# Kernel tuning notes

Hardware: AMD Instinct MI355X
Metric: run time of the kernel (lower is better)

## Reference

```python
import jax, jax.numpy as jnp
import numpy as np

B = 4096
N_PATCH = 196  # (28/2)^2


def _rx(theta):
    # theta [...] -> RX matrix [..., 2, 2] complex64
    c = jnp.cos(theta / 2) + 0j
    s = -1j * jnp.sin(theta / 2)
    return jnp.stack([jnp.stack([c, s], -1), jnp.stack([s, c], -1)], -2).astype(jnp.complex64)


def _rot(phi, theta, omega):
    # PennyLane Rot(phi, theta, omega) = RZ(omega) RY(theta) RZ(phi), returns [2,2] complex64
    ct = jnp.cos(theta / 2)
    st = jnp.sin(theta / 2)
    m00 = jnp.exp(-1j * (phi + omega) / 2) * ct
    m01 = -jnp.exp(1j * (phi - omega) / 2) * st
    m10 = jnp.exp(-1j * (phi - omega) / 2) * st
    m11 = jnp.exp(1j * (phi + omega) / 2) * ct
    return jnp.stack([jnp.stack([m00, m01]), jnp.stack([m10, m11])]).astype(jnp.complex64)


def _apply_shared(state, U, w):
    # state [N,2,2,2,2], U [2,2] shared across batch, acting on wire w
    s = jnp.moveaxis(state, 1 + w, -1)
    s = jnp.einsum('...a,ba->...b', s, U)
    return jnp.moveaxis(s, -1, 1 + w)


def _apply_batched(state, U, w):
    # U [N,2,2] per-sample gate
    s = jnp.moveaxis(state, 1 + w, -1)
    s = jnp.einsum('n...a,nba->n...b', s, U)
    return jnp.moveaxis(s, -1, 1 + w)


def _cnot(state, c, t):
    s = jnp.moveaxis(state, (1 + c, 1 + t), (-2, -1))
    s = jnp.stack([s[..., 0, :], s[..., 1, ::-1]], axis=-2)
    return jnp.moveaxis(s, (-2, -1), (1 + c, 1 + t))


def _quanv(patches, wq):
    # patches [N,4] angles; wq [n_app, n_layers, 4, 3]
    N = patches.shape[0]
    state = jnp.zeros((N, 16), jnp.complex64).at[:, 0].set(1.0).reshape(N, 2, 2, 2, 2)
    for w in range(4):  # AngleEmbedding: RX per wire
        state = _apply_batched(state, _rx(patches[:, w]), w)
    ranges = (1, 2)  # SEL default: (l % (n_wires-1)) + 1
    for app in range(wq.shape[0]):
        for l in range(wq.shape[1]):
            for w in range(4):
                state = _apply_shared(state, _rot(wq[app, l, w, 0], wq[app, l, w, 1], wq[app, l, w, 2]), w)
            r = ranges[l]
            for w in range(4):
                state = _cnot(state, w, (w + r) % 4)
    p = jnp.abs(state) ** 2  # [N,2,2,2,2]
    feats = []
    for w in range(4):  # <Z_w> = P(bit_w=0) - P(bit_w=1)
        axes = tuple(a for a in range(1, 5) if a != 1 + w)
        m = p.sum(axes)
        feats.append(m[:, 0] - m[:, 1])
    return jnp.stack(feats, -1)  # [N,4]


def _qfc(params, wfc):
    # 1-qubit circuit: RX embedding then Rot gates only (SEL has no entanglers on 1 wire)
    Bq = params.shape[0]
    state = jnp.zeros((Bq, 2), jnp.complex64).at[:, 0].set(1.0)
    state = jnp.einsum('na,nba->nb', state, _rx(params[:, 0]))
    for app in range(wfc.shape[0]):
        for l in range(wfc.shape[1]):
            U = _rot(wfc[app, l, 0, 0], wfc[app, l, 0, 1], wfc[app, l, 0, 2])
            state = jnp.einsum('na,ba->nb', state, U)
    p = jnp.abs(state) ** 2
    return p[:, 0] - p[:, 1]  # [B]


def setup_inputs() -> dict:
    key = jax.random.key(0)
    k1, k2, k3, k4 = jax.random.split(key, 4)
    return {
        'x': jax.random.normal(k1, (B, 784), jnp.float32),
        'weights_q': jax.random.normal(k2, (2, 2, 4, 3), jnp.float32),
        'weights_fc': jax.random.normal(k3, (3, 3, 1, 3), jnp.float32),
        'W_out': jax.random.normal(k4, (10, 1), jnp.float32) * 0.1,
        'b_out': jnp.zeros((10,), jnp.float32),
    }


def reference(x, weights_q, weights_fc, W_out, b_out):
    Bb = x.shape[0]
    img = x.reshape(Bb, 28, 28)
    # extract 2x2 stride-2 patches in (row-block, col-block) order, row-major within patch
    patches = img.reshape(Bb, 14, 2, 14, 2).transpose(0, 1, 3, 2, 4).reshape(Bb * N_PATCH, 4)
    feats = _quanv(patches, weights_q).reshape(Bb, N_PATCH * 4)  # [B,784]
    q = _qfc(feats[:, :1], weights_fc)  # [B]
    logits = q[:, None] @ W_out.T + b_out  # Linear(1,10) -> [B,10]
    return jax.nn.log_softmax(logits, axis=-1)
```

## Files before the change

kernel.cpp:

```cpp
#include <hip/hip_runtime.h>
#include <math.h>


struct c32 { float re, im; };

__device__ __forceinline__ c32 cmul(c32 a, c32 b) {
    return { fmaf(a.re, b.re, -a.im * b.im), fmaf(a.re, b.im, a.im * b.re) };
}
__device__ __forceinline__ c32 cadd(c32 a, c32 b) { return { a.re + b.re, a.im + b.im }; }

template<int W>
__device__ __forceinline__ void apply1(c32 amp[16], c32 u00, c32 u01, c32 u10, c32 u11) {
    constexpr int s = 8 >> W;
    #pragma unroll
    for (int i = 0; i < 16; ++i) {
        if (i & s) continue;
        c32 a = amp[i], b = amp[i + s];
        amp[i]     = cadd(cmul(u00, a), cmul(u01, b));
        amp[i + s] = cadd(cmul(u10, a), cmul(u11, b));
    }
}

template<int C, int T>
__device__ __forceinline__ void cnot4(c32 amp[16]) {
    constexpr int sc = 8 >> C, st = 8 >> T;
    #pragma unroll
    for (int i = 0; i < 16; ++i) {
        if ((i & sc) && !(i & st)) {
            c32 tmp = amp[i]; amp[i] = amp[i | st]; amp[i | st] = tmp;
        }
    }
}

__device__ __forceinline__ void make_rot(float phi, float th, float om,
                                         c32& u00, c32& u01, c32& u10, c32& u11) {
    float sh, ch; sincosf(th * 0.5f, &sh, &ch);
    float spo, cpo; sincosf((phi + om) * 0.5f, &spo, &cpo);
    float spm, cpm; sincosf((phi - om) * 0.5f, &spm, &cpm);
    u00 = {  cpo * ch, -spo * ch };
    u01 = { -cpm * sh, -spm * sh };
    u10 = {  cpm * sh, -spm * sh };
    u11 = {  cpo * ch,  spo * ch };
}

template<int W>
__device__ __forceinline__ void rx_apply(c32 amp[16], float ang) {
    float s, c; sincosf(ang * 0.5f, &s, &c);
    apply1<W>(amp, c32{c, 0.f}, c32{0.f, -s}, c32{0.f, -s}, c32{c, 0.f});
}

template<int W>
__device__ __forceinline__ void rot_apply(c32 amp[16], const float* p) {
    c32 a, b, c, d;
    make_rot(p[0], p[1], p[2], a, b, c, d);
    apply1<W>(amp, a, b, c, d);
}

__global__ __launch_bounds__(64)
void quanv_hybrid_kernel(const float* __restrict__ x,
                         const float* __restrict__ wq,
                         const float* __restrict__ wfc,
                         const float* __restrict__ Wout,
                         const float* __restrict__ bout,
                         float* __restrict__ out,
                         int B)
{
    int b = blockIdx.x * blockDim.x + threadIdx.x;
    if (b >= B) return;

    const float* xb = x + (size_t)b * 784;
    float ang0 = xb[0], ang1 = xb[1], ang2 = xb[28], ang3 = xb[29];

    c32 amp[16];
    #pragma unroll
    for (int i = 0; i < 16; ++i) amp[i] = { 0.f, 0.f };
    amp[0].re = 1.f;

    rx_apply<0>(amp, ang0);
    rx_apply<1>(amp, ang1);
    rx_apply<2>(amp, ang2);
    rx_apply<3>(amp, ang3);

    #pragma unroll
    for (int al = 0; al < 4; ++al) {
        const float* wp = wq + al * 12;
        rot_apply<0>(amp, wp + 0);
        rot_apply<1>(amp, wp + 3);
        rot_apply<2>(amp, wp + 6);
        rot_apply<3>(amp, wp + 9);
        if ((al & 1) == 0) {
            cnot4<0,1>(amp); cnot4<1,2>(amp); cnot4<2,3>(amp); cnot4<3,0>(amp);
        } else {
            cnot4<0,2>(amp); cnot4<1,3>(amp); cnot4<2,0>(amp); cnot4<3,1>(amp);
        }
    }

    float p0 = 0.f, p1 = 0.f;
    #pragma unroll
    for (int i = 0; i < 16; ++i) {
        float p = fmaf(amp[i].re, amp[i].re, amp[i].im * amp[i].im);
        if (i < 8) p0 += p; else p1 += p;
    }
    float z0 = p0 - p1;

    float sh, chh; sincosf(z0 * 0.5f, &sh, &chh);
    c32 psi0 = { chh, 0.f }, psi1 = { 0.f, -sh };
    #pragma unroll
    for (int g = 0; g < 9; ++g) {
        const float* p = wfc + g * 3;
        c32 u00, u01, u10, u11;
        make_rot(p[0], p[1], p[2], u00, u01, u10, u11);
        c32 n0 = cadd(cmul(u00, psi0), cmul(u01, psi1));
        c32 n1 = cadd(cmul(u10, psi0), cmul(u11, psi1));
        psi0 = n0; psi1 = n1;
    }
    float q = (psi0.re * psi0.re + psi0.im * psi0.im)
            - (psi1.re * psi1.re + psi1.im * psi1.im);

    float lg[10], m = -1e30f;
    #pragma unroll
    for (int j = 0; j < 10; ++j) {
        lg[j] = fmaf(q, Wout[j], bout[j]);
        m = fmaxf(m, lg[j]);
    }
    float sum = 0.f;
    #pragma unroll
    for (int j = 0; j < 10; ++j) sum += expf(lg[j] - m);
    float lse = m + logf(sum);

    float* ob = out + (size_t)b * 10;
    #pragma unroll
    for (int j = 0; j < 10; ++j) ob[j] = lg[j] - lse;
}

extern "C" void kernel_launch(void* const* d_in, const int* in_sizes, int n_in,
                              void* d_out, int out_size, void* d_ws, size_t ws_size,
                              hipStream_t stream) {
    const float* x    = (const float*)d_in[0];
    const float* wq   = (const float*)d_in[1];
    const float* wfc  = (const float*)d_in[2];
    const float* Wout = (const float*)d_in[3];
    const float* bout = (const float*)d_in[4];
    float* out = (float*)d_out;

    int B = in_sizes[0] / 784;
    const int threads = 64;
    int blocks = (B + threads - 1) / threads;
    quanv_hybrid_kernel<<<blocks, threads, 0, stream>>>(x, wq, wfc, Wout, bout, out, B);
}
```

Before: 86.21 us.

## Precompute circuit observable as Pauli-basis coefficients and evaluate per-sample polynomial

Each block first builds the 16x16 unitary of the weight layers in shared memory. It then forms the Z0 observable conjugated by that unitary, expands it into 81 Pauli-product coefficients, and collapses the 9-gate FC circuit into two scalars. Each sample now evaluates a small trigonometric polynomial in its four RX angles instead of simulating the full 16-amplitude state, which removes most of the per-sample complex arithmetic. In exchange every block recomputes the precomputation and adds three barriers, with block size raised to 256 threads.

```diff
diff --git a/kernel.cpp b/kernel.cpp
--- a/kernel.cpp
+++ b/kernel.cpp
@@ -8,29 +8,7 @@
     return { fmaf(a.re, b.re, -a.im * b.im), fmaf(a.re, b.im, a.im * b.re) };
 }
 __device__ __forceinline__ c32 cadd(c32 a, c32 b) { return { a.re + b.re, a.im + b.im }; }
-
-template<int W>
-__device__ __forceinline__ void apply1(c32 amp[16], c32 u00, c32 u01, c32 u10, c32 u11) {
-    constexpr int s = 8 >> W;
-    #pragma unroll
-    for (int i = 0; i < 16; ++i) {
-        if (i & s) continue;
-        c32 a = amp[i], b = amp[i + s];
-        amp[i]     = cadd(cmul(u00, a), cmul(u01, b));
-        amp[i + s] = cadd(cmul(u10, a), cmul(u11, b));
-    }
-}
-
-template<int C, int T>
-__device__ __forceinline__ void cnot4(c32 amp[16]) {
-    constexpr int sc = 8 >> C, st = 8 >> T;
-    #pragma unroll
-    for (int i = 0; i < 16; ++i) {
-        if ((i & sc) && !(i & st)) {
-            c32 tmp = amp[i]; amp[i] = amp[i | st]; amp[i | st] = tmp;
-        }
-    }
-}
+__device__ __forceinline__ c32 conjc(c32 a) { return { a.re, -a.im }; }
 
 __device__ __forceinline__ void make_rot(float phi, float th, float om,
                                          c32& u00, c32& u01, c32& u10, c32& u11) {
@@ -44,9 +22,26 @@
 }
 
 template<int W>
-__device__ __forceinline__ void rx_apply(c32 amp[16], float ang) {
-    float s, c; sincosf(ang * 0.5f, &s, &c);
-    apply1<W>(amp, c32{c, 0.f}, c32{0.f, -s}, c32{0.f, -s}, c32{c, 0.f});
+__device__ __forceinline__ void apply1(c32 amp[16], c32 u00, c32 u01, c32 u10, c32 u11) {
+    constexpr int s = 8 >> W;
+    #pragma unroll
+    for (int i = 0; i < 16; ++i) {
+        if (i & s) continue;
+        c32 a = amp[i], b = amp[i + s];
+        amp[i]     = cadd(cmul(u00, a), cmul(u01, b));
+        amp[i + s] = cadd(cmul(u10, a), cmul(u11, b));
+    }
+}
+
+template<int C, int T>
+__device__ __forceinline__ void cnot4(c32 amp[16]) {
+    constexpr int sc = 8 >> C, st = 8 >> T;
+    #pragma unroll
+    for (int i = 0; i < 16; ++i) {
+        if ((i & sc) && !(i & st)) {
+            c32 tmp = amp[i]; amp[i] = amp[i | st]; amp[i | st] = tmp;
+        }
+    }
 }
 
 template<int W>
@@ -56,7 +51,7 @@
     apply1<W>(amp, a, b, c, d);
 }
 
-__global__ __launch_bounds__(64)
+__global__ __launch_bounds__(256)
 void quanv_hybrid_kernel(const float* __restrict__ x,
                          const float* __restrict__ wq,
                          const float* __restrict__ wfc,
@@ -65,68 +60,142 @@
                          float* __restrict__ out,
                          int B)
 {
-    int b = blockIdx.x * blockDim.x + threadIdx.x;
+    __shared__ c32 U[16][16];
+    __shared__ c32 M[16][16];
+    __shared__ float mc[81];
+    __shared__ float fc_beta, fc_gamma;
+
+    const int tid = threadIdx.x;
+
+    if (tid < 16) {
+        c32 amp[16];
+        #pragma unroll
+        for (int i = 0; i < 16; ++i) amp[i] = { 0.f, 0.f };
+        amp[tid].re = 1.f;
+        #pragma unroll
+        for (int al = 0; al < 4; ++al) {
+            const float* wp = wq + al * 12;
+            rot_apply<0>(amp, wp + 0);
+            rot_apply<1>(amp, wp + 3);
+            rot_apply<2>(amp, wp + 6);
+            rot_apply<3>(amp, wp + 9);
+            if ((al & 1) == 0) {
+                cnot4<0,1>(amp); cnot4<1,2>(amp); cnot4<2,3>(amp); cnot4<3,0>(amp);
+            } else {
+                cnot4<0,2>(amp); cnot4<1,3>(amp); cnot4<2,0>(amp); cnot4<3,1>(amp);
+            }
+        }
+        #pragma unroll
+        for (int k = 0; k < 16; ++k) U[k][tid] = amp[k];
+    }
+
+    if (tid == 64) {
+        c32 v00 = {1.f,0.f}, v01 = {0.f,0.f}, v10 = {0.f,0.f}, v11 = {1.f,0.f};
+        #pragma unroll
+        for (int g = 0; g < 9; ++g) {
+            const float* p = wfc + g * 3;
+            c32 u00, u01, u10, u11;
+            make_rot(p[0], p[1], p[2], u00, u01, u10, u11);
+            c32 n00 = cadd(cmul(u00, v00), cmul(u01, v10));
+            c32 n01 = cadd(cmul(u00, v01), cmul(u01, v11));
+            c32 n10 = cadd(cmul(u10, v00), cmul(u11, v10));
+            c32 n11 = cadd(cmul(u10, v01), cmul(u11, v11));
+            v00 = n00; v01 = n01; v10 = n10; v11 = n11;
+        }
+        fc_beta  = (v00.re*v00.re + v00.im*v00.im) - (v10.re*v10.re + v10.im*v10.im);
+        c32 h01 = cadd(cmul(conjc(v00), v01),
+                       c32{ -(conjc(v10).re*v11.re - conjc(v10).im*v11.im),
+                            -(conjc(v10).re*v11.im + conjc(v10).im*v11.re) });
+        fc_gamma = h01.im;
+    }
+    __syncthreads();
+
+    {
+        const int i = tid >> 4, j = tid & 15;
+        c32 s = {0.f, 0.f};
+        #pragma unroll
+        for (int k = 0; k < 16; ++k) {
+            c32 t = cmul(conjc(U[k][i]), U[k][j]);
+            if (k < 8) { s.re += t.re; s.im += t.im; }
+            else       { s.re -= t.re; s.im -= t.im; }
+        }
+        M[i][j] = s;
+    }
+    __syncthreads();
+
+    if (tid < 81) {
+        const int t = tid;
+        int d[4] = { t / 27, (t / 9) % 3, (t / 3) % 3, t % 3 };
+        int xmask = 0;
+        #pragma unroll
+        for (int w = 0; w < 4; ++w) if (d[w] == 1) xmask |= (8 >> w);
+        float acc = 0.f;
+        float acci = 0.f;
+        for (int i = 0; i < 16; ++i) {
+            const int j = i ^ xmask;
+            float pre = 1.f, pim = 0.f;
+            #pragma unroll
+            for (int w = 0; w < 4; ++w) {
+                const int b = (i >> (3 - w)) & 1;
+                if (d[w] == 2) {
+                    if (b) { pre = -pre; pim = -pim; }
+                } else if (d[w] == 1) {
+                    float nre = b ? -pim :  pim;
+                    float nim = b ?  pre : -pre;
+                    pre = nre; pim = nim;
+                }
+            }
+            c32 m = M[j][i];
+            acc  += pre * m.re - pim * m.im;
+            acci += pre * m.im + pim * m.re;
+            (void)acci;
+        }
+        mc[t] = acc * (1.f / 16.f);
+    }
+    __syncthreads();
+
+    const int b = blockIdx.x * 256 + tid;
     if (b >= B) return;
 
     const float* xb = x + (size_t)b * 784;
-    float ang0 = xb[0], ang1 = xb[1], ang2 = xb[28], ang3 = xb[29];
-
-    c32 amp[16];
-    #pragma unroll
-    for (int i = 0; i < 16; ++i) amp[i] = { 0.f, 0.f };
-    amp[0].re = 1.f;
-
-    rx_apply<0>(amp, ang0);
-    rx_apply<1>(amp, ang1);
-    rx_apply<2>(amp, ang2);
-    rx_apply<3>(amp, ang3);
-
-    #pragma unroll
-    for (int al = 0; al < 4; ++al) {
-        const float* wp = wq + al * 12;
-        rot_apply<0>(amp, wp + 0);
-        rot_apply<1>(amp, wp + 3);
-        rot_apply<2>(amp, wp + 6);
-        rot_apply<3>(amp, wp + 9);
-        if ((al & 1) == 0) {
-            cnot4<0,1>(amp); cnot4<1,2>(amp); cnot4<2,3>(amp); cnot4<3,0>(amp);
-        } else {
-            cnot4<0,2>(amp); cnot4<1,3>(amp); cnot4<2,0>(amp); cnot4<3,1>(amp);
-        }
-    }
-
-    float p0 = 0.f, p1 = 0.f;
-    #pragma unroll
-    for (int i = 0; i < 16; ++i) {
-        float p = fmaf(amp[i].re, amp[i].re, amp[i].im * amp[i].im);
-        if (i < 8) p0 += p; else p1 += p;
-    }
-    float z0 = p0 - p1;
-
-    float sh, chh; sincosf(z0 * 0.5f, &sh, &chh);
-    c32 psi0 = { chh, 0.f }, psi1 = { 0.f, -sh };
-    #pragma unroll
-    for (int g = 0; g < 9; ++g) {
-        const float* p = wfc + g * 3;
-        c32 u00, u01, u10, u11;
-        make_rot(p[0], p[1], p[2], u00, u01, u10, u11);
-        c32 n0 = cadd(cmul(u00, psi0), cmul(u01, psi1));
-        c32 n1 = cadd(cmul(u10, psi0), cmul(u11, psi1));
-        psi0 = n0; psi1 = n1;
-    }
-    float q = (psi0.re * psi0.re + psi0.im * psi0.im)
-            - (psi1.re * psi1.re + psi1.im * psi1.im);
-
-    float lg[10], m = -1e30f;
+    const float a0 = xb[0], a1 = xb[1], a2 = xb[28], a3 = xb[29];
+
+    float u0[3], u1[3], u2[3], u3[3];
+    { float s, c; sincosf(a0, &s, &c); u0[0]=1.f; u0[1]=-s; u0[2]=c; }
+    { float s, c; sincosf(a1, &s, &c); u1[0]=1.f; u1[1]=-s; u1[2]=c; }
+    { float s, c; sincosf(a2, &s, &c); u2[0]=1.f; u2[1]=-s; u2[2]=c; }
+    { float s, c; sincosf(a3, &s, &c); u3[0]=1.f; u3[1]=-s; u3[2]=c; }
+
+    float z0 = 0.f;
+    #pragma unroll
+    for (int t0 = 0; t0 < 3; ++t0) {
+        float s1 = 0.f;
+        #pragma unroll
+        for (int t1 = 0; t1 < 3; ++t1) {
+            float s2 = 0.f;
+            #pragma unroll
+            for (int t2 = 0; t2 < 3; ++t2) {
+                const float* m = &mc[((t0 * 3 + t1) * 3 + t2) * 3];
+                s2 = fmaf(m[0] + fmaf(m[1], u3[1], 0.f) + m[2] * u3[2], u2[t2], s2);
+            }
+            s1 = fmaf(s2, u1[t1], s1);
+        }
+        z0 = fmaf(s1, u0[t0], z0);
+    }
+
+    float sz, cz; sincosf(z0, &sz, &cz);
+    const float q = fmaf(fc_beta, cz, fc_gamma * sz);
+
+    float lg[10], mx = -1e30f;
     #pragma unroll
     for (int j = 0; j < 10; ++j) {
         lg[j] = fmaf(q, Wout[j], bout[j]);
-        m = fmaxf(m, lg[j]);
+        mx = fmaxf(mx, lg[j]);
     }
     float sum = 0.f;
     #pragma unroll
-    for (int j = 0; j < 10; ++j) sum += expf(lg[j] - m);
-    float lse = m + logf(sum);
+    for (int j = 0; j < 10; ++j) sum += expf(lg[j] - mx);
+    const float lse = mx + logf(sum);
 
     float* ob = out + (size_t)b * 10;
     #pragma unroll
@@ -144,7 +213,6 @@
     float* out = (float*)d_out;
 
     int B = in_sizes[0] / 784;
-    const int threads = 64;
-    int blocks = (B + threads - 1) / threads;
-    quanv_hybrid_kernel<<<blocks, threads, 0, stream>>>(x, wq, wfc, Wout, bout, out, B);
-}
+    int blocks = (B + 255) / 256;
+    quanv_hybrid_kernel<<<blocks, 256, 0, stream>>>(x, wq, wfc, Wout, bout, out, B);
+}
```

Result: slower. 90.73 us (+5.2%).
